# Kernel optimization log

Measured on AMD Instinct MI355X. Metric: run time of the kernel, lower is better.

## Reference

```python
import jax, jax.numpy as jnp
import numpy as np

N, E = 20000, 320000
IN, HID, OUT, H = 128, 32, 1, 4
EPS = 1e-16  # PyG softmax epsilon


def _p(key, shape, scale=0.05):
    return jax.random.normal(key, shape, dtype=jnp.float32) * scale


def setup_inputs() -> dict:
    key = jax.random.key(0)
    ks = jax.random.split(key, 20)
    d = {
        "x": jax.random.normal(ks[0], (N, IN), dtype=jnp.float32),
        "edge_src": jax.random.randint(ks[1], (E,), 0, N, dtype=jnp.int32),
        "edge_dst": jax.random.randint(ks[2], (E,), 0, N, dtype=jnp.int32),
        # layer 1: TransformerConv(IN, HID, H)  ->  [N, H*HID]
        "W1q": _p(ks[3], (IN, H * HID)), "b1q": jnp.zeros((H * HID,), jnp.float32),
        "W1k": _p(ks[4], (IN, H * HID)), "b1k": jnp.zeros((H * HID,), jnp.float32),
        "W1v": _p(ks[5], (IN, H * HID)), "b1v": jnp.zeros((H * HID,), jnp.float32),
        "W1s": _p(ks[6], (IN, H * HID)), "b1s": jnp.zeros((H * HID,), jnp.float32),
        # layer 2: TransformerConv(H*HID, OUT, H) -> [N, H*OUT]
        "W2q": _p(ks[7], (H * HID, H * OUT)), "b2q": jnp.zeros((H * OUT,), jnp.float32),
        "W2k": _p(ks[8], (H * HID, H * OUT)), "b2k": jnp.zeros((H * OUT,), jnp.float32),
        "W2v": _p(ks[9], (H * HID, H * OUT)), "b2v": jnp.zeros((H * OUT,), jnp.float32),
        "W2s": _p(ks[10], (H * HID, H * OUT)), "b2s": jnp.zeros((H * OUT,), jnp.float32),
        # final nn.Linear(heads, 1)
        "Wl": _p(ks[11], (H, 1)), "bl": jnp.zeros((1,), jnp.float32),
    }
    return d


def transformer_conv(x, src, dst, Wq, bq, Wk, bk, Wv, bv, Ws, bs, heads, ch):
    n = x.shape[0]
    q = (x @ Wq + bq).reshape(n, heads, ch)
    k = (x @ Wk + bk).reshape(n, heads, ch)
    v = (x @ Wv + bv).reshape(n, heads, ch)
    qi, kj, vj = q[dst], k[src], v[src]            # [E,H,C] gathers
    score = (qi * kj).sum(-1) / jnp.sqrt(jnp.float32(ch))  # [E,H]
    m = jax.ops.segment_max(score, dst, num_segments=n)    # segment softmax by target
    e = jnp.exp(score - m[dst])
    s = jax.ops.segment_sum(e, dst, num_segments=n)
    alpha = e / (s[dst] + EPS)                              # [E,H]
    agg = jax.ops.segment_sum(alpha[:, :, None] * vj, dst, num_segments=n)  # [N,H,C]
    return agg.reshape(n, heads * ch) + x @ Ws + bs          # concat + root skip


def reference(x, edge_src, edge_dst,
              W1q, b1q, W1k, b1k, W1v, b1v, W1s, b1s,
              W2q, b2q, W2k, b2k, W2v, b2v, W2s, b2s,
              Wl, bl):
    h = transformer_conv(x, edge_src, edge_dst, W1q, b1q, W1k, b1k, W1v, b1v, W1s, b1s, H, HID)
    h = jax.nn.relu(h)  # dropout is identity in eval
    h = transformer_conv(h, edge_src, edge_dst, W2q, b2q, W2k, b2k, W2v, b2v, W2s, b2s, H, OUT)
    y = h @ Wl + bl                      # [N,1]
    return y.mean(axis=0, keepdims=True)  # [1,1]
```

## Files before the change

kernel.cpp:

```cpp
#include <hip/hip_runtime.h>
#include <math.h>

static constexpr float EPS_PYG = 1e-16f;
static constexpr float INV_SQRT32 = 0.17677669529663687f;

typedef short bf16x8 __attribute__((ext_vector_type(8)));
typedef float f32x4 __attribute__((ext_vector_type(4)));

__device__ inline unsigned short f2bf(float f) {
    union { float f; unsigned u; } x; x.f = f;
    unsigned r = x.u + 0x7FFFu + ((x.u >> 16) & 1u);
    return (unsigned short)(r >> 16);
}
__device__ inline float bf_hi(unsigned u) {
    union { unsigned u; float f; } x; x.u = u & 0xFFFF0000u; return x.f;
}
__device__ inline float bf_lo(unsigned u) {
    union { unsigned u; float f; } x; x.u = u << 16; return x.f;
}

__global__ __launch_bounds__(256) void build_prep_kernel(
    const int* __restrict__ dst, int* __restrict__ deg, int* __restrict__ slot,
    int E, int nblk_deg,
    const float4* __restrict__ X, ushort4* __restrict__ Xb, int total4,
    const float* __restrict__ Wq, const float* __restrict__ Wk,
    const float* __restrict__ Wv, const float* __restrict__ Wsk,
    unsigned short* __restrict__ Wbt)
{
    const int b = blockIdx.x;
    const int t = threadIdx.x;
    if (b < nblk_deg) {
        int e = b * 256 + t;
        if (e < E) slot[e] = atomicAdd(&deg[dst[e]], 1);
    } else if (b < nblk_deg + 4) {
        int m = b - nblk_deg;
        const float* W = (m == 0) ? Wq : (m == 1) ? Wk : (m == 2) ? Wv : Wsk;
        for (int i = t; i < 16384; i += 256) {
            int k = i >> 7, nn = i & 127;
            Wbt[m * 16384 + nn * 128 + k] = f2bf(W[i]);
        }
    } else {
        int i = (b - nblk_deg - 4) * 256 + t;
        if (i < total4) {
            float4 v = X[i];
            ushort4 o;
            o.x = f2bf(v.x); o.y = f2bf(v.y); o.z = f2bf(v.z); o.w = f2bf(v.w);
            Xb[i] = o;
        }
    }
}

__global__ __launch_bounds__(1024) void scan_kernel(const int* __restrict__ deg,
                                                    int* __restrict__ row_off, int n,
                                                    float* __restrict__ out,
                                                    const float* __restrict__ bl) {
    const int t = threadIdx.x;
    const int CH = (n + 1023) >> 10;
    const int base = t * CH;
    int vals[32];
    int sum = 0;
#pragma unroll 4
    for (int i = 0; i < CH; ++i) {
        int idx = base + i;
        int v = (idx < n) ? deg[idx] : 0;
        sum += v;
        vals[i] = sum;
    }
    const int lane = t & 63;
    const int wid = t >> 6;
    int wsum = sum;
#pragma unroll
    for (int off = 1; off < 64; off <<= 1) {
        int o = __shfl_up(wsum, off, 64);
        if (lane >= off) wsum += o;
    }
    __shared__ int wtot[16];
    if (lane == 63) wtot[wid] = wsum;
    __syncthreads();
    if (t < 64) {
        int v = (t < 16) ? wtot[t] : 0;
        int inc = v;
#pragma unroll
        for (int off = 1; off < 16; off <<= 1) {
            int o = __shfl_up(inc, off, 64);
            if (t >= off) inc += o;
        }
        if (t < 16) wtot[t] = inc - v;
    }
    __syncthreads();
    const int toff = wtot[wid] + (wsum - sum);
    if (t == 0) { row_off[0] = 0; out[0] = bl[0]; }
#pragma unroll 4
    for (int i = 0; i < CH; ++i) {
        int idx = base + i;
        if (idx < n) row_off[idx + 1] = toff + vals[i];
    }
}

__global__ void scatter_kernel(const int* __restrict__ src, const int* __restrict__ dst,
                               const int* __restrict__ row_off, const int* __restrict__ slot,
                               int* __restrict__ csr_src, int E) {
    int e = blockIdx.x * blockDim.x + threadIdx.x;
    if (e < E) csr_src[row_off[dst[e]] + slot[e]] = src[e];
}

__global__ __launch_bounds__(256) void gemm1_mfma(
    const unsigned short* __restrict__ Xb, const unsigned short* __restrict__ Wbt,
    const float* __restrict__ bq, const float* __restrict__ bk,
    const float* __restrict__ bv, const float* __restrict__ bsk,
    float* __restrict__ Q, unsigned int* __restrict__ KV,
    float* __restrict__ S, int n)
{
    const int mode = blockIdx.y;

    const int tid  = threadIdx.x;
    const int wave = tid >> 6;
    const int lane = tid & 63;
    const int m    = lane & 15;
    const int quad = lane >> 4;
    const int r0   = blockIdx.x * 64 + wave * 16;

    int arow = r0 + m;
    if (arow >= n) arow = n - 1;

    if (mode == 1) {
        const unsigned short* WK = Wbt + 16384;
        const unsigned short* WV = Wbt + 2 * 16384;
        f32x4 accK[8] = {};
        f32x4 accV[8] = {};
#pragma unroll
        for (int kc = 0; kc < 128; kc += 32) {
            bf16x8 a = *(const bf16x8*)(Xb + (size_t)arow * 128 + kc + quad * 8);
#pragma unroll
            for (int ct = 0; ct < 8; ++ct) {
                bf16x8 bk8 = *(const bf16x8*)(WK + (ct * 16 + m) * 128 + kc + quad * 8);
                accK[ct] = __builtin_amdgcn_mfma_f32_16x16x32_bf16(a, bk8, accK[ct], 0, 0, 0);
                bf16x8 bv8 = *(const bf16x8*)(WV + (ct * 16 + m) * 128 + kc + quad * 8);
                accV[ct] = __builtin_amdgcn_mfma_f32_16x16x32_bf16(a, bv8, accV[ct], 0, 0, 0);
            }
        }
#pragma unroll
        for (int ct = 0; ct < 8; ++ct) {
            const int col = ct * 16 + m;
            const float bbk = bk[col], bbv = bv[col];
#pragma unroll
            for (int r = 0; r < 4; ++r) {
                const int row = r0 + quad * 4 + r;
                if (row < n) {
                    unsigned kb = f2bf(accK[ct][r] + bbk);
                    unsigned vb = f2bf(accV[ct][r] + bbv);
                    KV[(size_t)row * 128 + col] = (kb << 16) | vb;
                }
            }
        }
    } else {
        const int mat = (mode == 0) ? 0 : 3;
        const unsigned short* W = Wbt + (size_t)mat * 16384;
        const float* bias = (mode == 0) ? bq : bsk;
        float* C = (mode == 0) ? Q : S;
        f32x4 acc[8] = {};
#pragma unroll
        for (int kc = 0; kc < 128; kc += 32) {
            bf16x8 a = *(const bf16x8*)(Xb + (size_t)arow * 128 + kc + quad * 8);
#pragma unroll
            for (int ct = 0; ct < 8; ++ct) {
                bf16x8 bfr = *(const bf16x8*)(W + (ct * 16 + m) * 128 + kc + quad * 8);
                acc[ct] = __builtin_amdgcn_mfma_f32_16x16x32_bf16(a, bfr, acc[ct], 0, 0, 0);
            }
        }
#pragma unroll
        for (int ct = 0; ct < 8; ++ct) {
            const int col = ct * 16 + m;
            const float bb = bias[col];
#pragma unroll
            for (int r = 0; r < 4; ++r) {
                const int row = r0 + quad * 4 + r;
                if (row < n) C[(size_t)row * 128 + col] = acc[ct][r] + bb;
            }
        }
    }
}

__global__ __launch_bounds__(256) void l1_agg_kernel(
    const float* __restrict__ Q, const unsigned int* __restrict__ KV,
    const float* __restrict__ S,
    const int* __restrict__ row_off, const int* __restrict__ csr_src,
    float* __restrict__ H1, int n)
{
    const int t = threadIdx.x;
    const int node = blockIdx.x * 4 + (t >> 6);
    if (node >= n) return;
    const int l    = t & 31;
    const int half = (t >> 5) & 1;
    const int cbase = ((l >> 3) << 5) + ((l & 7) << 2);

    const float4 q = *(const float4*)(Q + (size_t)node * 128 + cbase);
    const int beg = row_off[node], end = row_off[node + 1];

    float lsum = 0.f, a0 = 0.f, a1 = 0.f, a2 = 0.f, a3 = 0.f;
    int pos = beg + half;
    for (; pos + 2 < end; pos += 4) {
        int s0 = csr_src[pos];
        int s1 = csr_src[pos + 2];
        uint4 u0 = *(const uint4*)(KV + (size_t)s0 * 128 + cbase);
        uint4 u1 = *(const uint4*)(KV + (size_t)s1 * 128 + cbase);
        float p0 = q.x * bf_hi(u0.x) + q.y * bf_hi(u0.y)
                 + q.z * bf_hi(u0.z) + q.w * bf_hi(u0.w);
        float p1 = q.x * bf_hi(u1.x) + q.y * bf_hi(u1.y)
                 + q.z * bf_hi(u1.z) + q.w * bf_hi(u1.w);
        p0 += __shfl_xor(p0, 4, 8);  p1 += __shfl_xor(p1, 4, 8);
        p0 += __shfl_xor(p0, 2, 8);  p1 += __shfl_xor(p1, 2, 8);
        p0 += __shfl_xor(p0, 1, 8);  p1 += __shfl_xor(p1, 1, 8);
        float e0 = __expf(p0 * INV_SQRT32);
        float e1 = __expf(p1 * INV_SQRT32);
        lsum += e0 + e1;
        a0 += e0 * bf_lo(u0.x) + e1 * bf_lo(u1.x);
        a1 += e0 * bf_lo(u0.y) + e1 * bf_lo(u1.y);
        a2 += e0 * bf_lo(u0.z) + e1 * bf_lo(u1.z);
        a3 += e0 * bf_lo(u0.w) + e1 * bf_lo(u1.w);
    }
    if (pos < end) {
        int s0 = csr_src[pos];
        uint4 u0 = *(const uint4*)(KV + (size_t)s0 * 128 + cbase);
        float p0 = q.x * bf_hi(u0.x) + q.y * bf_hi(u0.y)
                 + q.z * bf_hi(u0.z) + q.w * bf_hi(u0.w);
        p0 += __shfl_xor(p0, 4, 8);
        p0 += __shfl_xor(p0, 2, 8);
        p0 += __shfl_xor(p0, 1, 8);
        float e0 = __expf(p0 * INV_SQRT32);
        lsum += e0;
        a0 += e0 * bf_lo(u0.x);
        a1 += e0 * bf_lo(u0.y);
        a2 += e0 * bf_lo(u0.z);
        a3 += e0 * bf_lo(u0.w);
    }
    lsum += __shfl_xor(lsum, 32, 64);
    a0   += __shfl_xor(a0,   32, 64);
    a1   += __shfl_xor(a1,   32, 64);
    a2   += __shfl_xor(a2,   32, 64);
    a3   += __shfl_xor(a3,   32, 64);
    if (half == 0) {
        const float inv = 1.0f / (lsum + EPS_PYG);
        const float4 sk = *(const float4*)(S + (size_t)node * 128 + cbase);
        float4 o;
        o.x = fmaxf(a0 * inv + sk.x, 0.f);
        o.y = fmaxf(a1 * inv + sk.y, 0.f);
        o.z = fmaxf(a2 * inv + sk.z, 0.f);
        o.w = fmaxf(a3 * inv + sk.w, 0.f);
        *(float4*)(H1 + (size_t)node * 128 + cbase) = o;
    }
}

__global__ __launch_bounds__(256) void gemm2_kernel(
    const float* __restrict__ H1,
    const float* __restrict__ Wq, const float* __restrict__ Wk,
    const float* __restrict__ Wv, const float* __restrict__ Wsk,
    const float* __restrict__ bq, const float* __restrict__ bk,
    const float* __restrict__ bv, const float* __restrict__ bsk,
    float4* __restrict__ Q2, float4* __restrict__ KV2, float4* __restrict__ S2, int n)
{
    __shared__ float Hs[64][129];
    __shared__ float Wt[128][16];
    __shared__ float bt[16];

    const int tid = threadIdx.x;
    const int r0 = blockIdx.x * 64;

    for (int i = tid; i < 2048; i += 256) {
        int row = i >> 4, col = i & 15;
        int mt = col >> 2, c = col & 3;
        const float* Wm = (mt == 0) ? Wq : (mt == 1) ? Wk : (mt == 2) ? Wv : Wsk;
        Wt[row][col] = Wm[row * 4 + c];
    }
    if (tid < 16) {
        int mt = tid >> 2;
        const float* bm = (mt == 0) ? bq : (mt == 1) ? bk : (mt == 2) ? bv : bsk;
        bt[tid] = bm[tid & 3];
    }
    for (int f = tid; f < 2048; f += 256) {
        int row = f >> 5, c4 = f & 31;
        float4 val = make_float4(0.f, 0.f, 0.f, 0.f);
        if (r0 + row < n) val = ((const float4*)H1)[(size_t)(r0 + row) * 32 + c4];
        Hs[row][c4 * 4 + 0] = val.x;
        Hs[row][c4 * 4 + 1] = val.y;
        Hs[row][c4 * 4 + 2] = val.z;
        Hs[row][c4 * 4 + 3] = val.w;
    }
    __syncthreads();

    const int nl = tid & 63;
    const int jg = tid >> 6;
    float a0 = 0.f, a1 = 0.f, a2 = 0.f, a3 = 0.f;
#pragma unroll 4
    for (int k = 0; k < 128; ++k) {
        float h = Hs[nl][k];
        a0 += h * Wt[k][jg * 4 + 0];
        a1 += h * Wt[k][jg * 4 + 1];
        a2 += h * Wt[k][jg * 4 + 2];
        a3 += h * Wt[k][jg * 4 + 3];
    }
    int node = r0 + nl;
    if (node < n) {
        float4 o = make_float4(a0 + bt[jg * 4 + 0], a1 + bt[jg * 4 + 1],
                               a2 + bt[jg * 4 + 2], a3 + bt[jg * 4 + 3]);
        if (jg == 0)      Q2[node] = o;
        else if (jg == 1) KV2[(size_t)node * 2 + 0] = o;
        else if (jg == 2) KV2[(size_t)node * 2 + 1] = o;
        else              S2[node] = o;
    }
}

__global__ __launch_bounds__(256) void l2_agg_kernel(
    const float4* __restrict__ Q2, const float4* __restrict__ KV2,
    const float4* __restrict__ S2,
    const int* __restrict__ row_off, const int* __restrict__ csr_src,
    const float* __restrict__ Wl, float* __restrict__ out, int n, float invn)
{
    const int t  = threadIdx.x;
    const int g  = t >> 4;
    const int gl = t & 15;
    const int nd = blockIdx.x * 16 + g;
    float y = 0.f;
    if (nd < n) {
        const int beg = row_off[nd], end = row_off[nd + 1];
        float4 q = Q2[nd];
        float l0 = 0.f, l1 = 0.f, l2 = 0.f, l3 = 0.f;
        float a0 = 0.f, a1 = 0.f, a2 = 0.f, a3 = 0.f;
        for (int pos = beg + gl; pos < end; pos += 16) {
            int src = csr_src[pos];
            float4 k = KV2[(size_t)src * 2 + 0];
            float4 v = KV2[(size_t)src * 2 + 1];
            float e0 = __expf(q.x * k.x);
            float e1 = __expf(q.y * k.y);
            float e2 = __expf(q.z * k.z);
            float e3 = __expf(q.w * k.w);
            l0 += e0; a0 += e0 * v.x;
            l1 += e1; a1 += e1 * v.y;
            l2 += e2; a2 += e2 * v.z;
            l3 += e3; a3 += e3 * v.w;
        }
#pragma unroll
        for (int mk = 8; mk >= 1; mk >>= 1) {
            l0 += __shfl_xor(l0, mk, 16); l1 += __shfl_xor(l1, mk, 16);
            l2 += __shfl_xor(l2, mk, 16); l3 += __shfl_xor(l3, mk, 16);
            a0 += __shfl_xor(a0, mk, 16); a1 += __shfl_xor(a1, mk, 16);
            a2 += __shfl_xor(a2, mk, 16); a3 += __shfl_xor(a3, mk, 16);
        }
        if (gl == 0) {
            float4 sk = S2[nd];
            float h0 = a0 / (l0 + EPS_PYG) + sk.x;
            float h1 = a1 / (l1 + EPS_PYG) + sk.y;
            float h2 = a2 / (l2 + EPS_PYG) + sk.z;
            float h3 = a3 / (l3 + EPS_PYG) + sk.w;
            y = (h0 * Wl[0] + h1 * Wl[1] + h2 * Wl[2] + h3 * Wl[3]) * invn;
        }
    }
    __shared__ float red[256];
    red[t] = y;
    __syncthreads();
    for (int off = 128; off > 0; off >>= 1) {
        if (t < (unsigned)off) red[t] += red[t + off];
        __syncthreads();
    }
    if (t == 0) atomicAdd(out, red[0]);
}

extern "C" void kernel_launch(void* const* d_in, const int* in_sizes, int n_in,
                              void* d_out, int out_size, void* d_ws, size_t ws_size,
                              hipStream_t stream) {
    const float* x        = (const float*)d_in[0];
    const int*   edge_src = (const int*)d_in[1];
    const int*   edge_dst = (const int*)d_in[2];
    const float* W1q = (const float*)d_in[3];  const float* b1q = (const float*)d_in[4];
    const float* W1k = (const float*)d_in[5];  const float* b1k = (const float*)d_in[6];
    const float* W1v = (const float*)d_in[7];  const float* b1v = (const float*)d_in[8];
    const float* W1s = (const float*)d_in[9];  const float* b1s = (const float*)d_in[10];
    const float* W2q = (const float*)d_in[11]; const float* b2q = (const float*)d_in[12];
    const float* W2k = (const float*)d_in[13]; const float* b2k = (const float*)d_in[14];
    const float* W2v = (const float*)d_in[15]; const float* b2v = (const float*)d_in[16];
    const float* W2s = (const float*)d_in[17]; const float* b2s = (const float*)d_in[18];
    const float* Wl  = (const float*)d_in[19]; const float* bl  = (const float*)d_in[20];

    const int N = in_sizes[0] / 128;
    const int E = in_sizes[1];
    float* out = (float*)d_out;

    float* ws  = (float*)d_ws;
    size_t off = 0;
    float*        Q1  = ws + off; off += (size_t)N * 128;
    unsigned int* KV  = (unsigned int*)(ws + off); off += (size_t)N * 128;
    float*        S1  = ws + off; off += (size_t)N * 128;
    float*        H1  = ws + off; off += (size_t)N * 128;
    float*        q2  = ws + off; off += (size_t)N * 4;
    float*        kv2 = ws + off; off += (size_t)N * 8;
    float*        s2  = ws + off; off += (size_t)N * 4;
    unsigned short* Xb  = (unsigned short*)(ws + off); off += (size_t)N * 64;
    unsigned short* Wbt = (unsigned short*)(ws + off); off += 4 * 16384 / 2;
    int* ibase   = (int*)(ws + off);
    int* deg     = ibase;
    int* row_off = ibase + N;
    int* slot    = ibase + 2 * N + 4;
    int* csr_src = slot + E;

    const int nblk_e = (E + 255) / 256;
    const int total4 = N * 32;
    const int nblk_x = (total4 + 255) / 256;
    const int nblk_g = (N + 63) / 64;

    hipMemsetAsync(deg, 0, (size_t)N * sizeof(int), stream);
    build_prep_kernel<<<nblk_e + 4 + nblk_x, 256, 0, stream>>>(
        edge_dst, deg, slot, E, nblk_e,
        (const float4*)x, (ushort4*)Xb, total4, W1q, W1k, W1v, W1s, Wbt);
    scan_kernel<<<1, 1024, 0, stream>>>(deg, row_off, N, out, bl);
    scatter_kernel<<<nblk_e, 256, 0, stream>>>(edge_src, edge_dst, row_off,
                                               slot, csr_src, E);
    {
        dim3 grid(nblk_g, 3);
        gemm1_mfma<<<grid, 256, 0, stream>>>(Xb, Wbt, b1q, b1k, b1v, b1s,
                                             Q1, KV, S1, N);
    }
    l1_agg_kernel<<<(N + 3) / 4, 256, 0, stream>>>(Q1, KV, S1, row_off, csr_src, H1, N);
    gemm2_kernel<<<nblk_g, 256, 0, stream>>>(H1, W2q, W2k, W2v, W2s,
                                             b2q, b2k, b2v, b2s,
                                             (float4*)q2, (float4*)kv2,
                                             (float4*)s2, N);
    l2_agg_kernel<<<(N + 15) / 16, 256, 0, stream>>>((const float4*)q2,
                                                     (const float4*)kv2,
                                                     (const float4*)s2,
                                                     row_off, csr_src, Wl, out, N,
                                                     1.0f / (float)N);
}
```

Measured before the change: 234.3 us.

## Fuse layer-2 projection GEMM into layer-1 aggregation kernel

Merges the layer-1 attention aggregation and the small layer-2 QKVS projection into one kernel. Each wave computes a node's 128-wide hidden row, stages it in shared memory, and immediately multiplies it by the 128x16 layer-2 weights held in LDS. This removes one kernel launch and the write and re-read of the N x 128 H1 buffer. In exchange, every block of 4 nodes reloads the full 2048-element weight matrix into LDS, adding a barrier and redundant loads per block.

```diff
diff --git a/kernel.cpp b/kernel.cpp
--- a/kernel.cpp
+++ b/kernel.cpp
@@ -181,132 +181,119 @@
     }
 }
 
-__global__ __launch_bounds__(256) void l1_agg_kernel(
+__global__ __launch_bounds__(256) void l1_fused_kernel(
     const float* __restrict__ Q, const unsigned int* __restrict__ KV,
     const float* __restrict__ S,
     const int* __restrict__ row_off, const int* __restrict__ csr_src,
-    float* __restrict__ H1, int n)
+    const float* __restrict__ W2q, const float* __restrict__ W2k,
+    const float* __restrict__ W2v, const float* __restrict__ W2s,
+    const float* __restrict__ b2q, const float* __restrict__ b2k,
+    const float* __restrict__ b2v, const float* __restrict__ b2s,
+    float4* __restrict__ q2, float4* __restrict__ kv2, float4* __restrict__ s2,
+    int n)
 {
+    __shared__ float Wt[128][17];
+    __shared__ float bt[16];
+    __shared__ float hrow[4][132];
+
     const int t = threadIdx.x;
-    const int node = blockIdx.x * 4 + (t >> 6);
-    if (node >= n) return;
-    const int l    = t & 31;
-    const int half = (t >> 5) & 1;
-    const int cbase = ((l >> 3) << 5) + ((l & 7) << 2);
-
-    const float4 q = *(const float4*)(Q + (size_t)node * 128 + cbase);
-    const int beg = row_off[node], end = row_off[node + 1];
-
-    float lsum = 0.f, a0 = 0.f, a1 = 0.f, a2 = 0.f, a3 = 0.f;
-    int pos = beg + half;
-    for (; pos + 2 < end; pos += 4) {
-        int s0 = csr_src[pos];
-        int s1 = csr_src[pos + 2];
-        uint4 u0 = *(const uint4*)(KV + (size_t)s0 * 128 + cbase);
-        uint4 u1 = *(const uint4*)(KV + (size_t)s1 * 128 + cbase);
-        float p0 = q.x * bf_hi(u0.x) + q.y * bf_hi(u0.y)
-                 + q.z * bf_hi(u0.z) + q.w * bf_hi(u0.w);
-        float p1 = q.x * bf_hi(u1.x) + q.y * bf_hi(u1.y)
-                 + q.z * bf_hi(u1.z) + q.w * bf_hi(u1.w);
-        p0 += __shfl_xor(p0, 4, 8);  p1 += __shfl_xor(p1, 4, 8);
-        p0 += __shfl_xor(p0, 2, 8);  p1 += __shfl_xor(p1, 2, 8);
-        p0 += __shfl_xor(p0, 1, 8);  p1 += __shfl_xor(p1, 1, 8);
-        float e0 = __expf(p0 * INV_SQRT32);
-        float e1 = __expf(p1 * INV_SQRT32);
-        lsum += e0 + e1;
-        a0 += e0 * bf_lo(u0.x) + e1 * bf_lo(u1.x);
-        a1 += e0 * bf_lo(u0.y) + e1 * bf_lo(u1.y);
-        a2 += e0 * bf_lo(u0.z) + e1 * bf_lo(u1.z);
-        a3 += e0 * bf_lo(u0.w) + e1 * bf_lo(u1.w);
-    }
-    if (pos < end) {
-        int s0 = csr_src[pos];
-        uint4 u0 = *(const uint4*)(KV + (size_t)s0 * 128 + cbase);
-        float p0 = q.x * bf_hi(u0.x) + q.y * bf_hi(u0.y)
-                 + q.z * bf_hi(u0.z) + q.w * bf_hi(u0.w);
-        p0 += __shfl_xor(p0, 4, 8);
-        p0 += __shfl_xor(p0, 2, 8);
-        p0 += __shfl_xor(p0, 1, 8);
-        float e0 = __expf(p0 * INV_SQRT32);
-        lsum += e0;
-        a0 += e0 * bf_lo(u0.x);
-        a1 += e0 * bf_lo(u0.y);
-        a2 += e0 * bf_lo(u0.z);
-        a3 += e0 * bf_lo(u0.w);
-    }
-    lsum += __shfl_xor(lsum, 32, 64);
-    a0   += __shfl_xor(a0,   32, 64);
-    a1   += __shfl_xor(a1,   32, 64);
-    a2   += __shfl_xor(a2,   32, 64);
-    a3   += __shfl_xor(a3,   32, 64);
-    if (half == 0) {
-        const float inv = 1.0f / (lsum + EPS_PYG);
-        const float4 sk = *(const float4*)(S + (size_t)node * 128 + cbase);
-        float4 o;
-        o.x = fmaxf(a0 * inv + sk.x, 0.f);
-        o.y = fmaxf(a1 * inv + sk.y, 0.f);
-        o.z = fmaxf(a2 * inv + sk.z, 0.f);
-        o.w = fmaxf(a3 * inv + sk.w, 0.f);
-        *(float4*)(H1 + (size_t)node * 128 + cbase) = o;
-    }
-}
-
-__global__ __launch_bounds__(256) void gemm2_kernel(
-    const float* __restrict__ H1,
-    const float* __restrict__ Wq, const float* __restrict__ Wk,
-    const float* __restrict__ Wv, const float* __restrict__ Wsk,
-    const float* __restrict__ bq, const float* __restrict__ bk,
-    const float* __restrict__ bv, const float* __restrict__ bsk,
-    float4* __restrict__ Q2, float4* __restrict__ KV2, float4* __restrict__ S2, int n)
-{
-    __shared__ float Hs[64][129];
-    __shared__ float Wt[128][16];
-    __shared__ float bt[16];
-
-    const int tid = threadIdx.x;
-    const int r0 = blockIdx.x * 64;
-
-    for (int i = tid; i < 2048; i += 256) {
+
+    for (int i = t; i < 2048; i += 256) {
         int row = i >> 4, col = i & 15;
         int mt = col >> 2, c = col & 3;
-        const float* Wm = (mt == 0) ? Wq : (mt == 1) ? Wk : (mt == 2) ? Wv : Wsk;
+        const float* Wm = (mt == 0) ? W2q : (mt == 1) ? W2k : (mt == 2) ? W2v : W2s;
         Wt[row][col] = Wm[row * 4 + c];
     }
-    if (tid < 16) {
-        int mt = tid >> 2;
-        const float* bm = (mt == 0) ? bq : (mt == 1) ? bk : (mt == 2) ? bv : bsk;
-        bt[tid] = bm[tid & 3];
-    }
-    for (int f = tid; f < 2048; f += 256) {
-        int row = f >> 5, c4 = f & 31;
-        float4 val = make_float4(0.f, 0.f, 0.f, 0.f);
-        if (r0 + row < n) val = ((const float4*)H1)[(size_t)(r0 + row) * 32 + c4];
-        Hs[row][c4 * 4 + 0] = val.x;
-        Hs[row][c4 * 4 + 1] = val.y;
-        Hs[row][c4 * 4 + 2] = val.z;
-        Hs[row][c4 * 4 + 3] = val.w;
+    if (t < 16) {
+        int mt = t >> 2;
+        const float* bm = (mt == 0) ? b2q : (mt == 1) ? b2k : (mt == 2) ? b2v : b2s;
+        bt[t] = bm[t & 3];
     }
     __syncthreads();
 
-    const int nl = tid & 63;
-    const int jg = tid >> 6;
-    float a0 = 0.f, a1 = 0.f, a2 = 0.f, a3 = 0.f;
-#pragma unroll 4
-    for (int k = 0; k < 128; ++k) {
-        float h = Hs[nl][k];
-        a0 += h * Wt[k][jg * 4 + 0];
-        a1 += h * Wt[k][jg * 4 + 1];
-        a2 += h * Wt[k][jg * 4 + 2];
-        a3 += h * Wt[k][jg * 4 + 3];
-    }
-    int node = r0 + nl;
+    const int w    = t >> 6;
+    const int lane = t & 63;
+    const int node = blockIdx.x * 4 + w;
+
     if (node < n) {
-        float4 o = make_float4(a0 + bt[jg * 4 + 0], a1 + bt[jg * 4 + 1],
-                               a2 + bt[jg * 4 + 2], a3 + bt[jg * 4 + 3]);
-        if (jg == 0)      Q2[node] = o;
-        else if (jg == 1) KV2[(size_t)node * 2 + 0] = o;
-        else if (jg == 2) KV2[(size_t)node * 2 + 1] = o;
-        else              S2[node] = o;
+        const int l    = lane & 31;
+        const int half = (lane >> 5) & 1;
+        const int cbase = ((l >> 3) << 5) + ((l & 7) << 2);
+
+        const float4 q = *(const float4*)(Q + (size_t)node * 128 + cbase);
+        const int beg = row_off[node], end = row_off[node + 1];
+        float lsum = 0.f, a0 = 0.f, a1 = 0.f, a2 = 0.f, a3 = 0.f;
+        int pos = beg + half;
+        for (; pos + 2 < end; pos += 4) {
+            int s0 = csr_src[pos];
+            int s1 = csr_src[pos + 2];
+            uint4 u0 = *(const uint4*)(KV + (size_t)s0 * 128 + cbase);
+            uint4 u1 = *(const uint4*)(KV + (size_t)s1 * 128 + cbase);
+            float p0 = q.x * bf_hi(u0.x) + q.y * bf_hi(u0.y)
+                     + q.z * bf_hi(u0.z) + q.w * bf_hi(u0.w);
+            float p1 = q.x * bf_hi(u1.x) + q.y * bf_hi(u1.y)
+                     + q.z * bf_hi(u1.z) + q.w * bf_hi(u1.w);
+            p0 += __shfl_xor(p0, 4, 8);  p1 += __shfl_xor(p1, 4, 8);
+            p0 += __shfl_xor(p0, 2, 8);  p1 += __shfl_xor(p1, 2, 8);
+            p0 += __shfl_xor(p0, 1, 8);  p1 += __shfl_xor(p1, 1, 8);
+            float e0 = __expf(p0 * INV_SQRT32);
+            float e1 = __expf(p1 * INV_SQRT32);
+            lsum += e0 + e1;
+            a0 += e0 * bf_lo(u0.x) + e1 * bf_lo(u1.x);
+            a1 += e0 * bf_lo(u0.y) + e1 * bf_lo(u1.y);
+            a2 += e0 * bf_lo(u0.z) + e1 * bf_lo(u1.z);
+            a3 += e0 * bf_lo(u0.w) + e1 * bf_lo(u1.w);
+        }
+        if (pos < end) {
+            int s0 = csr_src[pos];
+            uint4 u0 = *(const uint4*)(KV + (size_t)s0 * 128 + cbase);
+            float p0 = q.x * bf_hi(u0.x) + q.y * bf_hi(u0.y)
+                     + q.z * bf_hi(u0.z) + q.w * bf_hi(u0.w);
+            p0 += __shfl_xor(p0, 4, 8);
+            p0 += __shfl_xor(p0, 2, 8);
+            p0 += __shfl_xor(p0, 1, 8);
+            float e0 = __expf(p0 * INV_SQRT32);
+            lsum += e0;
+            a0 += e0 * bf_lo(u0.x);
+            a1 += e0 * bf_lo(u0.y);
+            a2 += e0 * bf_lo(u0.z);
+            a3 += e0 * bf_lo(u0.w);
+        }
+        lsum += __shfl_xor(lsum, 32, 64);
+        a0   += __shfl_xor(a0,   32, 64);
+        a1   += __shfl_xor(a1,   32, 64);
+        a2   += __shfl_xor(a2,   32, 64);
+        a3   += __shfl_xor(a3,   32, 64);
+        if (half == 0) {
+            const float inv = 1.0f / (lsum + EPS_PYG);
+            const float4 sk = *(const float4*)(S + (size_t)node * 128 + cbase);
+            float4 o;
+            o.x = fmaxf(a0 * inv + sk.x, 0.f);
+            o.y = fmaxf(a1 * inv + sk.y, 0.f);
+            o.z = fmaxf(a2 * inv + sk.z, 0.f);
+            o.w = fmaxf(a3 * inv + sk.w, 0.f);
+            *(float4*)&hrow[w][cbase] = o;
+        }
+
+        const int oc = lane & 15;
+        const int ck = lane >> 4;
+        const float* h = &hrow[w][ck * 32];
+        float r = 0.f;
+#pragma unroll
+        for (int jj = 0; jj < 32; ++jj) {
+            int j = (jj + ck * 8) & 31;
+            r += h[j] * Wt[ck * 32 + j][oc];
+        }
+        r += __shfl_xor(r, 16, 64);
+        r += __shfl_xor(r, 32, 64);
+        if (lane < 16) {
+            float val = r + bt[oc];
+            int mt = oc >> 2, cc = oc & 3;
+            if (mt == 0)      ((float*)q2)[(size_t)node * 4 + cc] = val;
+            else if (mt == 1) ((float*)kv2)[(size_t)node * 8 + cc] = val;
+            else if (mt == 2) ((float*)kv2)[(size_t)node * 8 + 4 + cc] = val;
+            else              ((float*)s2)[(size_t)node * 4 + cc] = val;
+        }
     }
 }
 
@@ -390,7 +377,6 @@
     float*        Q1  = ws + off; off += (size_t)N * 128;
     unsigned int* KV  = (unsigned int*)(ws + off); off += (size_t)N * 128;
     float*        S1  = ws + off; off += (size_t)N * 128;
-    float*        H1  = ws + off; off += (size_t)N * 128;
     float*        q2  = ws + off; off += (size_t)N * 4;
     float*        kv2 = ws + off; off += (size_t)N * 8;
     float*        s2  = ws + off; off += (size_t)N * 4;
@@ -419,11 +405,10 @@
         gemm1_mfma<<<grid, 256, 0, stream>>>(Xb, Wbt, b1q, b1k, b1v, b1s,
                                              Q1, KV, S1, N);
     }
-    l1_agg_kernel<<<(N + 3) / 4, 256, 0, stream>>>(Q1, KV, S1, row_off, csr_src, H1, N);
-    gemm2_kernel<<<nblk_g, 256, 0, stream>>>(H1, W2q, W2k, W2v, W2s,
-                                             b2q, b2k, b2v, b2s,
-                                             (float4*)q2, (float4*)kv2,
-                                             (float4*)s2, N);
+    l1_fused_kernel<<<(N + 3) / 4, 256, 0, stream>>>(
+        Q1, KV, S1, row_off, csr_src,
+        W2q, W2k, W2v, W2s, b2q, b2k, b2v, b2s,
+        (float4*)q2, (float4*)kv2, (float4*)s2, N);
     l2_agg_kernel<<<(N + 15) / 16, 256, 0, stream>>>((const float4*)q2,
                                                      (const float4*)kv2,
                                                      (const float4*)s2,
```

New measurement: 235.5 us. About the same (+0.5%).
